# Optimization experiments

Hardware: AMD Instinct MI355X
Metric: run time of the kernel (lower is better)

Reference implementation:

```python
import jax, jax.numpy as jnp
import numpy as np

B, T, I, H = 64, 512, 1024, 1024

def setup_inputs() -> dict:
    key = jax.random.key(0)
    ks = jax.random.split(key, 9)
    def xavier(k, shape):
        bound = np.sqrt(6.0 / (shape[0] + shape[1])).astype(np.float32)
        return jax.random.uniform(k, shape, jnp.float32, -bound, bound)
    inp = {"x": jax.random.normal(ks[0], (B, T, I), jnp.float32)}
    names = ["W_ii", "W_hi", "W_if", "W_hf", "W_ig", "W_hg", "W_io", "W_ho"]
    for n, k in zip(names, ks[1:]):
        rows = I if n[2] == "i" else H
        inp[n] = xavier(k, (rows, H))
    for n in ["b_ii", "b_hi", "b_if", "b_hf", "b_ig", "b_hg", "b_io", "b_ho"]:
        inp[n] = jnp.zeros((H,), jnp.float32)
    return inp

def _lstm(x, W_ii, b_ii, W_hi, b_hi, W_if, b_if, W_hf, b_hf,
          W_ig, b_ig, W_hg, b_hg, W_io, b_io, W_ho, b_ho):
    Bsz, Tlen, _ = x.shape
    Hdim = W_ii.shape[1]
    # Fuse 4 input-side and 4 hidden-side GEMMs into two big ones (same math).
    Wx = jnp.concatenate([W_if, W_ii, W_ig, W_io], axis=1)  # [I, 4H]
    Wh = jnp.concatenate([W_hf, W_hi, W_hg, W_ho], axis=1)  # [H, 4H]
    bsum = jnp.concatenate([b_if + b_hf, b_ii + b_hi, b_ig + b_hg, b_io + b_ho])
    # Hoist the input projection out of the recurrence: [T, B, 4H]
    xg = jnp.swapaxes(jnp.einsum('bti,ig->btg', x, Wx) + bsum, 0, 1)

    def step(carry, g_in):
        h, c = carry
        g = g_in + h @ Wh  # [B, 4H]
        f = jax.nn.sigmoid(g[:, :Hdim])
        i = jax.nn.sigmoid(g[:, Hdim:2 * Hdim])
        gt = jnp.tanh(g[:, 2 * Hdim:3 * Hdim])
        o = jax.nn.sigmoid(g[:, 3 * Hdim:])  # module uses sigmoid_it here
        c_new = f * c + i * gt
        h_new = jnp.tanh(c_new) * o
        return (h_new, c_new), None

    h0 = jnp.zeros((Bsz, Hdim), x.dtype)
    c0 = jnp.zeros((Bsz, Hdim), x.dtype)
    (h_t, c_t), _ = jax.lax.scan(step, (h0, c0), xg)
    return h_t, c_t

def reference(x, W_ii, b_ii, W_hi, b_hi, W_if, b_if, W_hf, b_hf,
              W_ig, b_ig, W_hg, b_hg, W_io, b_io, W_ho, b_ho):
    return _lstm(x, W_ii, b_ii, W_hi, b_hi, W_if, b_if, W_hf, b_hf,
                 W_ig, b_ig, W_hg, b_hg, W_io, b_io, W_ho, b_ho)
```

## Files before the change

### kernel.cpp

```cpp
#include <hip/hip_runtime.h>
#include <hip/hip_bf16.h>

typedef unsigned short u16;
typedef unsigned int   u32;
typedef unsigned long long u64;
typedef short short8 __attribute__((ext_vector_type(8)));
typedef float f32x4  __attribute__((ext_vector_type(4)));
typedef u16   u16x4  __attribute__((ext_vector_type(4)));

#define T_STEPS 512
#define BATCH   64
#define HD      1024
#define NBLK    128
#define NTHR    256
#define NCOL    32
#define WKS     2056
#define HBUF_E  (BATCH * HD)

#define W_BYTES    (NCOL * WKS * 2)
#define G_OFF      W_BYTES
#define G_STRIDE   33
#define G_BYTES    (BATCH * G_STRIDE * 4)
#define B_OFF      (G_OFF + G_BYTES)
#define B_BYTES    (NCOL * 4)
#define F_OFF      (B_OFF + B_BYTES)
#define SMEM_BYTES (F_OFF + 16)

__device__ __forceinline__ float sigm(float x) { return 1.f / (1.f + __expf(-x)); }
__device__ __forceinline__ float tanh_(float x) {
    float ax = __builtin_fabsf(x);
    float e  = __expf(-2.f * ax);
    float r  = (1.f - e) / (1.f + e);
    return x < 0.f ? -r : r;
}
__device__ __forceinline__ short bfb(float f) {
    __hip_bfloat16 h = __float2bfloat16(f);
    return *(short*)&h;
}

__device__ int detect_bf16(const u32* __restrict__ x) {
    int c = 0;
#pragma unroll 8
    for (int i = 0; i < 256; ++i) {
        u32 e = (x[i] >> 7) & 0xFF;
        c += (e >= 100 && e <= 140) ? 1 : 0;
    }
    return c >= 128;
}

extern "C" __global__ void __launch_bounds__(256)
cvt_x_kernel(const void* __restrict__ x, u16* __restrict__ xb, int n4)
{
    __shared__ int flg;
    if (threadIdx.x == 0) flg = detect_bf16((const u32*)x);
    __syncthreads();
    if (flg) return;
    const float4* xf = (const float4*)x;
    u16x4* xo = (u16x4*)xb;
    for (int i = blockIdx.x * blockDim.x + threadIdx.x; i < n4;
         i += gridDim.x * blockDim.x) {
        float4 v = xf[i];
        u16x4 o;
        o[0] = (u16)bfb(v.x); o[1] = (u16)bfb(v.y);
        o[2] = (u16)bfb(v.z); o[3] = (u16)bfb(v.w);
        xo[i] = o;
    }
}

union Frag16 { u64 q[2]; short8 s8[1]; };

__device__ __forceinline__ void load_chunk_atomic(const u16* hp, int c, Frag16* buf) {
#pragma unroll
    for (int it = 0; it < 4; ++it) {
        const u16* ptr = hp + c * 128 + it * 32;
        buf[it].q[0] = __hip_atomic_load((const u64*)ptr, __ATOMIC_RELAXED,
                                         __HIP_MEMORY_SCOPE_AGENT);
        buf[it].q[1] = __hip_atomic_load((const u64*)(ptr + 4), __ATOMIC_RELAXED,
                                         __HIP_MEMORY_SCOPE_AGENT);
    }
}

#define LDX(dst, base, OFFSTR) \
    asm volatile("global_load_dwordx4 %0, %1, off offset:" OFFSTR \
                 : "=v"(dst) : "v"(base))

#define ISSUE_CHUNK(ci) do {                                            \
    const int cc_ = (c0 + (ci)) & 7;                                    \
    u64 bA_ = (u64)(hp + (size_t)cc_ * 8192) + 4096;                    \
    u64 bB_ = bA_ + 8192;                                               \
    LDX(buf[ci][0], bA_, "-4096"); LDX(buf[ci][1], bA_, "0");           \
    LDX(buf[ci][2], bB_, "-4096"); LDX(buf[ci][3], bB_, "0");           \
} while (0)

#define HCHUNK(ci, VMSTR) do {                                          \
    asm volatile("s_waitcnt vmcnt(" VMSTR ")");                         \
    __builtin_amdgcn_sched_barrier(0);                                  \
    const int cc_ = (c0 + (ci)) & 7;                                    \
    const u16* wA_ = wb0 + 1024 + cc_ * 128;                            \
    const u16* wB_ = wb1 + 1024 + cc_ * 128;                            \
    short8 b0_, b1_;                                                    \
    b0_ = *(const short8*)(wA_);       b1_ = *(const short8*)(wB_);     \
    a0 = __builtin_amdgcn_mfma_f32_16x16x32_bf16(buf[ci][0], b0_, a0, 0, 0, 0); \
    a1 = __builtin_amdgcn_mfma_f32_16x16x32_bf16(buf[ci][0], b1_, a1, 0, 0, 0); \
    b0_ = *(const short8*)(wA_ + 32);  b1_ = *(const short8*)(wB_ + 32);\
    a0 = __builtin_amdgcn_mfma_f32_16x16x32_bf16(buf[ci][1], b0_, a0, 0, 0, 0); \
    a1 = __builtin_amdgcn_mfma_f32_16x16x32_bf16(buf[ci][1], b1_, a1, 0, 0, 0); \
    b0_ = *(const short8*)(wA_ + 64);  b1_ = *(const short8*)(wB_ + 64);\
    a0 = __builtin_amdgcn_mfma_f32_16x16x32_bf16(buf[ci][2], b0_, a0, 0, 0, 0); \
    a1 = __builtin_amdgcn_mfma_f32_16x16x32_bf16(buf[ci][2], b1_, a1, 0, 0, 0); \
    b0_ = *(const short8*)(wA_ + 96);  b1_ = *(const short8*)(wB_ + 96);\
    a0 = __builtin_amdgcn_mfma_f32_16x16x32_bf16(buf[ci][3], b0_, a0, 0, 0, 0); \
    a1 = __builtin_amdgcn_mfma_f32_16x16x32_bf16(buf[ci][3], b1_, a1, 0, 0, 0); \
} while (0)

extern "C" __global__ void __launch_bounds__(NTHR, 1)
lstm_persistent(const void* __restrict__ x,
                const void* __restrict__ Wxf, const void* __restrict__ Wxi,
                const void* __restrict__ Wxg, const void* __restrict__ Wxo,
                const void* __restrict__ Whf, const void* __restrict__ Whi,
                const void* __restrict__ Whg, const void* __restrict__ Who,
                const void* __restrict__ bxf, const void* __restrict__ bxi,
                const void* __restrict__ bxg, const void* __restrict__ bxo,
                const void* __restrict__ bhf, const void* __restrict__ bhi,
                const void* __restrict__ bhg, const void* __restrict__ bho,
                u16* __restrict__ hring, int ring_on,
                u16* __restrict__ xb, int* __restrict__ flags,
                void* __restrict__ outv)
{
    __builtin_amdgcn_fence(__ATOMIC_ACQUIRE, "agent");

    extern __shared__ char smem[];
    u16*   w_lds = (u16*)smem;
    float* g_lds = (float*)(smem + G_OFF);
    float* b_lds = (float*)(smem + B_OFF);
    int*   f_lds = (int*)(smem + F_OFF);

    const int tid = threadIdx.x;
    const int blk = blockIdx.x;

    if (tid == 0) f_lds[0] = detect_bf16((const u32*)x);
    __syncthreads();
    const int bf16mode = f_lds[0];

    {
        const int gate = tid >> 6;
        const int kb   = tid & 63;
        const void* WX[4] = {Wxf, Wxi, Wxg, Wxo};
        const void* WH[4] = {Whf, Whi, Whg, Who};
        for (int it = 0; it < 16; ++it) {
            int k = it * 64 + kb;
            u16 vx[8], vh[8];
            if (bf16mode) {
                short8 a = *(const short8*)((const u16*)WX[gate] + (size_t)k * HD + blk * 8);
                short8 b = *(const short8*)((const u16*)WH[gate] + (size_t)k * HD + blk * 8);
#pragma unroll
                for (int ci = 0; ci < 8; ++ci) { vx[ci] = (u16)a[ci]; vh[ci] = (u16)b[ci]; }
            } else {
                const float* px = (const float*)WX[gate] + (size_t)k * HD + blk * 8;
                const float* ph = (const float*)WH[gate] + (size_t)k * HD + blk * 8;
                float4 a0 = *(const float4*)px, a1 = *(const float4*)(px + 4);
                float4 b0 = *(const float4*)ph, b1 = *(const float4*)(ph + 4);
                vx[0]=(u16)bfb(a0.x); vx[1]=(u16)bfb(a0.y); vx[2]=(u16)bfb(a0.z); vx[3]=(u16)bfb(a0.w);
                vx[4]=(u16)bfb(a1.x); vx[5]=(u16)bfb(a1.y); vx[6]=(u16)bfb(a1.z); vx[7]=(u16)bfb(a1.w);
                vh[0]=(u16)bfb(b0.x); vh[1]=(u16)bfb(b0.y); vh[2]=(u16)bfb(b0.z); vh[3]=(u16)bfb(b0.w);
                vh[4]=(u16)bfb(b1.x); vh[5]=(u16)bfb(b1.y); vh[6]=(u16)bfb(b1.z); vh[7]=(u16)bfb(b1.w);
            }
#pragma unroll
            for (int ci = 0; ci < 8; ++ci) {
                w_lds[(gate * 8 + ci) * WKS + k]        = vx[ci];
                w_lds[(gate * 8 + ci) * WKS + 1024 + k] = vh[ci];
            }
        }
    }
    if (tid < NCOL) {
        const void* BX[4] = {bxf, bxi, bxg, bxo};
        const void* BH[4] = {bhf, bhi, bhg, bho};
        int gate = tid >> 3, hc = blk * 8 + (tid & 7);
        float v;
        if (bf16mode)
            v = __bfloat162float(((const __hip_bfloat16*)BX[gate])[hc]) +
                __bfloat162float(((const __hip_bfloat16*)BH[gate])[hc]);
        else
            v = ((const float*)BX[gate])[hc] + ((const float*)BH[gate])[hc];
        b_lds[tid] = v;
    }
    __syncthreads();

    const int wv   = tid >> 6;
    const int lane = tid & 63;
    const int c16  = lane & 15;
    const int quad = lane >> 4;
    const int arow = wv * 16 + c16;

    const int use16 = bf16mode || (xb != nullptr);
    const u16*   x16l = nullptr;
    const float* xf_l = nullptr;
    if (use16) {
        const u16* x16 = bf16mode ? (const u16*)x : xb;
        x16l = x16 + (size_t)arow * T_STEPS * HD + quad * 8;
    } else {
        xf_l = (const float*)x + (size_t)arow * T_STEPS * HD + quad * 8;
    }
    const u16* wb0 = w_lds + c16 * WKS + quad * 8;
    const u16* wb1 = w_lds + (16 + c16) * WKS + quad * 8;

    const int grow = wv * 16 + (lane >> 2);
    const int hl0  = (lane & 3) * 2;
    float bias[8];
#pragma unroll
    for (int g = 0; g < 4; ++g) {
        bias[g * 2]     = b_lds[g * 8 + hl0];
        bias[g * 2 + 1] = b_lds[g * 8 + hl0 + 1];
    }
    float creg[2] = {0.f, 0.f};

    const int c0 = blk >> 4;

    f32x4 ax0 = {0.f,0.f,0.f,0.f}, ax1 = {0.f,0.f,0.f,0.f};
    if (use16) {
        const u16* xp = x16l;
#pragma unroll 8
        for (int kc = 0; kc < 32; ++kc) {
            short8 a  = *(const short8*)(xp + kc * 32);
            short8 b0 = *(const short8*)(wb0 + kc * 32);
            short8 b1 = *(const short8*)(wb1 + kc * 32);
            ax0 = __builtin_amdgcn_mfma_f32_16x16x32_bf16(a, b0, ax0, 0, 0, 0);
            ax1 = __builtin_amdgcn_mfma_f32_16x16x32_bf16(a, b1, ax1, 0, 0, 0);
        }
    } else {
        const float* xp = xf_l;
#pragma unroll 4
        for (int kc = 0; kc < 32; ++kc) {
            float4 fa = *(const float4*)(xp + kc * 32);
            float4 fb = *(const float4*)(xp + kc * 32 + 4);
            short8 a = {bfb(fa.x), bfb(fa.y), bfb(fa.z), bfb(fa.w),
                        bfb(fb.x), bfb(fb.y), bfb(fb.z), bfb(fb.w)};
            short8 b0 = *(const short8*)(wb0 + kc * 32);
            short8 b1 = *(const short8*)(wb1 + kc * 32);
            ax0 = __builtin_amdgcn_mfma_f32_16x16x32_bf16(a, b0, ax0, 0, 0, 0);
            ax1 = __builtin_amdgcn_mfma_f32_16x16x32_bf16(a, b1, ax1, 0, 0, 0);
        }
    }

    for (int t = 0; t < T_STEPS; ++t) {
        f32x4 a0 = ax0, a1 = ax1;

        if (t > 0) {
            while (true) {
                int f1 = __hip_atomic_load(&flags[4 * lane + wv], __ATOMIC_RELAXED,
                                           __HIP_MEMORY_SCOPE_AGENT);
                int f2 = __hip_atomic_load(&flags[256 + 4 * lane + wv], __ATOMIC_RELAXED,
                                           __HIP_MEMORY_SCOPE_AGENT);
                u64 m1 = __ballot(f1 >= t);
                u64 m2 = __ballot(f2 >= t);
                if ((m1 & m2) == ~0ull) break;
                __builtin_amdgcn_s_sleep(1);
            }
            asm volatile("" ::: "memory");

            if (ring_on) {
                const u16* hp = hring + (size_t)(t - 1) * HBUF_E
                              + quad * 512 + arow * 8;
                short8 buf[8][4];
                asm volatile("s_waitcnt vmcnt(0)");
                ISSUE_CHUNK(0); ISSUE_CHUNK(1); ISSUE_CHUNK(2); ISSUE_CHUNK(3);
                ISSUE_CHUNK(4); ISSUE_CHUNK(5); ISSUE_CHUNK(6); ISSUE_CHUNK(7);
                HCHUNK(0, "28"); HCHUNK(1, "24"); HCHUNK(2, "20"); HCHUNK(3, "16");
                HCHUNK(4, "12"); HCHUNK(5, "8");  HCHUNK(6, "4");  HCHUNK(7, "0");
            } else {
                const u16* hp = hring + (size_t)(t & 1) * HBUF_E
                              + (size_t)arow * HD + quad * 8;
                Frag16 bufc[4];
                for (int ci = 0; ci < 8; ++ci) {
                    const int cc = (c0 + ci) & 7;
                    load_chunk_atomic(hp, cc, bufc);
#pragma unroll
                    for (int it = 0; it < 4; ++it) {
                        short8 a  = bufc[it].s8[0];
                        short8 b0 = *(const short8*)(wb0 + 1024 + cc * 128 + it * 32);
                        short8 b1 = *(const short8*)(wb1 + 1024 + cc * 128 + it * 32);
                        a0 = __builtin_amdgcn_mfma_f32_16x16x32_bf16(a, b0, a0, 0, 0, 0);
                        a1 = __builtin_amdgcn_mfma_f32_16x16x32_bf16(a, b1, a1, 0, 0, 0);
                    }
                }
            }
        }

        const int rr = wv * 16 + quad * 4;
#pragma unroll
        for (int i2 = 0; i2 < 4; ++i2) {
            g_lds[(rr + i2) * G_STRIDE + c16]      = a0[i2];
            g_lds[(rr + i2) * G_STRIDE + 16 + c16] = a1[i2];
        }
        asm volatile("s_waitcnt lgkmcnt(0)" ::: "memory");

        float hv[2], cv[2];
#pragma unroll
        for (int jj = 0; jj < 2; ++jj) {
            int hl = hl0 + jj;
            float gf = g_lds[grow * G_STRIDE + hl]      + bias[jj];
            float gi = g_lds[grow * G_STRIDE + 8 + hl]  + bias[2 + jj];
            float gg = g_lds[grow * G_STRIDE + 16 + hl] + bias[4 + jj];
            float go = g_lds[grow * G_STRIDE + 24 + hl] + bias[6 + jj];
            float fg = sigm(gf), ig = sigm(gi), og = sigm(go);
            float gt = tanh_(gg);
            float cnew = fg * creg[jj] + ig * gt;
            creg[jj] = cnew;
            cv[jj] = cnew;
            hv[jj] = tanh_(cnew) * og;
        }

        if (t < T_STEPS - 1) {
            u32 pk = (u32)(u16)bfb(hv[0]) | ((u32)(u16)bfb(hv[1]) << 16);
            if (ring_on) {
                u16* hn = hring + (size_t)t * HBUF_E;
                __hip_atomic_store((u32*)(hn + (size_t)blk * 512 + grow * 8 + hl0),
                                   pk, __ATOMIC_RELAXED, __HIP_MEMORY_SCOPE_AGENT);
            } else {
                u16* hn = hring + (size_t)((t + 1) & 1) * HBUF_E;
                __hip_atomic_store((u32*)(hn + (size_t)grow * HD + blk * 8 + hl0),
                                   pk, __ATOMIC_RELAXED, __HIP_MEMORY_SCOPE_AGENT);
            }
            asm volatile("s_waitcnt vmcnt(0)" ::: "memory");
            if (lane == 0)
                __hip_atomic_store(&flags[4 * blk + wv], t + 1, __ATOMIC_RELAXED,
                                   __HIP_MEMORY_SCOPE_AGENT);

            ax0 = (f32x4){0.f,0.f,0.f,0.f};
            ax1 = (f32x4){0.f,0.f,0.f,0.f};
            if (use16) {
                const u16* xp = x16l + (size_t)(t + 1) * HD;
#pragma unroll 8
                for (int kc = 0; kc < 32; ++kc) {
                    short8 a  = *(const short8*)(xp + kc * 32);
                    short8 b0 = *(const short8*)(wb0 + kc * 32);
                    short8 b1 = *(const short8*)(wb1 + kc * 32);
                    ax0 = __builtin_amdgcn_mfma_f32_16x16x32_bf16(a, b0, ax0, 0, 0, 0);
                    ax1 = __builtin_amdgcn_mfma_f32_16x16x32_bf16(a, b1, ax1, 0, 0, 0);
                }
            } else {
                const float* xp = xf_l + (size_t)(t + 1) * HD;
#pragma unroll 4
                for (int kc = 0; kc < 32; ++kc) {
                    float4 fa = *(const float4*)(xp + kc * 32);
                    float4 fb = *(const float4*)(xp + kc * 32 + 4);
                    short8 a = {bfb(fa.x), bfb(fa.y), bfb(fa.z), bfb(fa.w),
                                bfb(fb.x), bfb(fb.y), bfb(fb.z), bfb(fb.w)};
                    short8 b0 = *(const short8*)(wb0 + kc * 32);
                    short8 b1 = *(const short8*)(wb1 + kc * 32);
                    ax0 = __builtin_amdgcn_mfma_f32_16x16x32_bf16(a, b0, ax0, 0, 0, 0);
                    ax1 = __builtin_amdgcn_mfma_f32_16x16x32_bf16(a, b1, ax1, 0, 0, 0);
                }
            }
        } else {
#pragma unroll
            for (int jj = 0; jj < 2; ++jj) {
                size_t idx = (size_t)grow * HD + blk * 8 + hl0 + jj;
                if (bf16mode) {
                    u16* o = (u16*)outv;
                    __hip_bfloat16 hb = __float2bfloat16(hv[jj]);
                    __hip_bfloat16 cb = __float2bfloat16(cv[jj]);
                    o[idx] = *(u16*)&hb;
                    o[(size_t)BATCH * HD + idx] = *(u16*)&cb;
                } else {
                    float* o = (float*)outv;
                    o[idx] = hv[jj];
                    o[(size_t)BATCH * HD + idx] = cv[jj];
                }
            }
        }
    }
}

extern "C" void kernel_launch(void* const* d_in, const int* in_sizes, int n_in,
                              void* d_out, int out_size, void* d_ws, size_t ws_size,
                              hipStream_t stream) {
    (void)in_sizes; (void)n_in; (void)out_size;
    const void* x   = d_in[0];
    const void* Wii = d_in[1];  const void* Whi = d_in[2];
    const void* Wif = d_in[3];  const void* Whf = d_in[4];
    const void* Wig = d_in[5];  const void* Whg = d_in[6];
    const void* Wio = d_in[7];  const void* Who = d_in[8];
    const void* bii = d_in[9];  const void* bhi = d_in[10];
    const void* bif = d_in[11]; const void* bhf = d_in[12];
    const void* big = d_in[13]; const void* bhg = d_in[14];
    const void* bio = d_in[15]; const void* bho = d_in[16];

    int* flags = (int*)d_ws;
    u16* hring = (u16*)((char*)d_ws + 4096);

    const size_t ring_bytes = (size_t)T_STEPS * HBUF_E * 2;
    const size_t xb_bytes   = (size_t)BATCH * T_STEPS * HD * 2;
    int ring_on = 0;
    u16* xb = nullptr;
    if (ws_size >= 4096 + ring_bytes + xb_bytes) {
        ring_on = 1;
        xb = (u16*)((char*)d_ws + 4096 + ring_bytes);
    } else if (ws_size >= 4096 + ring_bytes) {
        ring_on = 1;
    } else if (ws_size >= 4096 + (size_t)2 * HBUF_E * 2 + xb_bytes) {
        xb = (u16*)((char*)d_ws + 4096 + (size_t)2 * HBUF_E * 2);
    }

    hipMemsetAsync(d_ws, 0, 4096, stream);
    if (xb)
        hipLaunchKernelGGL(cvt_x_kernel, dim3(2048), dim3(256), 0, stream,
                           x, xb, (BATCH * T_STEPS * HD) / 4);

    hipFuncSetAttribute((const void*)lstm_persistent,
                        hipFuncAttributeMaxDynamicSharedMemorySize, SMEM_BYTES);
    hipLaunchKernelGGL(lstm_persistent, dim3(NBLK), dim3(NTHR), SMEM_BYTES, stream,
                       x, Wif, Wii, Wig, Wio, Whf, Whi, Whg, Who,
                       bif, bii, big, bio, bhf, bhi, bhg, bho,
                       hring, ring_on, xb, flags, d_out);
}
```

Before: 4.753 ms.

## Replace flag polling with poisoned-ring data validation for hidden-state sync

In ring mode the per-step flag spin-wait and flag stores are removed. A pre-kernel fills the hidden-state ring with a poison pattern, and consumers speculatively load h chunks, checking each for poison. Clean chunks go straight into the MFMAs, and dirty chunks are reloaded atomically until valid. This takes the flag round-trip off the per-step critical path. The cost is a 64MB poison fill before the kernel, and correctness depends on no valid bf16 pair matching the poison pattern and on 32-bit stores landing atomically.

Measured after the change: 5.822 ms. 1.22x slower.

```diff
diff --git a/kernel.cpp b/kernel.cpp
--- a/kernel.cpp
+++ b/kernel.cpp
@@ -7,6 +7,7 @@
 typedef short short8 __attribute__((ext_vector_type(8)));
 typedef float f32x4  __attribute__((ext_vector_type(4)));
 typedef u16   u16x4  __attribute__((ext_vector_type(4)));
+typedef u32   u32x4  __attribute__((ext_vector_type(4)));
 
 #define T_STEPS 512
 #define BATCH   64
@@ -16,6 +17,7 @@
 #define NCOL    32
 #define WKS     2056
 #define HBUF_E  (BATCH * HD)
+#define POISON  0xFFFFFFFFu
 
 #define W_BYTES    (NCOL * WKS * 2)
 #define G_OFF      W_BYTES
@@ -67,7 +69,17 @@
     }
 }
 
+extern "C" __global__ void __launch_bounds__(256)
+poison_ring_kernel(u32x4* __restrict__ ring, long n)
+{
+    u32x4 p = {POISON, POISON, POISON, POISON};
+    for (long i = (long)blockIdx.x * blockDim.x + threadIdx.x; i < n;
+         i += (long)gridDim.x * blockDim.x)
+        ring[i] = p;
+}
+
 union Frag16 { u64 q[2]; short8 s8[1]; };
+union HF     { short8 s8; u32 w[4]; u64 q[2]; };
 
 __device__ __forceinline__ void load_chunk_atomic(const u16* hp, int c, Frag16* buf) {
 #pragma unroll
@@ -80,6 +92,16 @@
     }
 }
 
+__device__ __forceinline__ int chunk_clean(const HF* b) {
+    u32 ok = 1;
+#pragma unroll
+    for (int it = 0; it < 4; ++it)
+#pragma unroll
+        for (int d = 0; d < 4; ++d)
+            ok &= (b[it].w[d] != POISON) ? 1u : 0u;
+    return __all((int)ok);
+}
+
 #define LDX(dst, base, OFFSTR) \
     asm volatile("global_load_dwordx4 %0, %1, off offset:" OFFSTR \
                  : "=v"(dst) : "v"(base))
@@ -88,29 +110,34 @@
     const int cc_ = (c0 + (ci)) & 7;                                    \
     u64 bA_ = (u64)(hp + (size_t)cc_ * 8192) + 4096;                    \
     u64 bB_ = bA_ + 8192;                                               \
-    LDX(buf[ci][0], bA_, "-4096"); LDX(buf[ci][1], bA_, "0");           \
-    LDX(buf[ci][2], bB_, "-4096"); LDX(buf[ci][3], bB_, "0");           \
+    LDX(buf[ci][0].s8, bA_, "-4096"); LDX(buf[ci][1].s8, bA_, "0");     \
+    LDX(buf[ci][2].s8, bB_, "-4096"); LDX(buf[ci][3].s8, bB_, "0");     \
 } while (0)
 
-#define HCHUNK(ci, VMSTR) do {                                          \
-    asm volatile("s_waitcnt vmcnt(" VMSTR ")");                         \
-    __builtin_amdgcn_sched_barrier(0);                                  \
+#define MFMA_CHUNK(ci) do {                                             \
     const int cc_ = (c0 + (ci)) & 7;                                    \
     const u16* wA_ = wb0 + 1024 + cc_ * 128;                            \
     const u16* wB_ = wb1 + 1024 + cc_ * 128;                            \
     short8 b0_, b1_;                                                    \
     b0_ = *(const short8*)(wA_);       b1_ = *(const short8*)(wB_);     \
-    a0 = __builtin_amdgcn_mfma_f32_16x16x32_bf16(buf[ci][0], b0_, a0, 0, 0, 0); \
-    a1 = __builtin_amdgcn_mfma_f32_16x16x32_bf16(buf[ci][0], b1_, a1, 0, 0, 0); \
+    a0 = __builtin_amdgcn_mfma_f32_16x16x32_bf16(buf[ci][0].s8, b0_, a0, 0, 0, 0); \
+    a1 = __builtin_amdgcn_mfma_f32_16x16x32_bf16(buf[ci][0].s8, b1_, a1, 0, 0, 0); \
     b0_ = *(const short8*)(wA_ + 32);  b1_ = *(const short8*)(wB_ + 32);\
-    a0 = __builtin_amdgcn_mfma_f32_16x16x32_bf16(buf[ci][1], b0_, a0, 0, 0, 0); \
-    a1 = __builtin_amdgcn_mfma_f32_16x16x32_bf16(buf[ci][1], b1_, a1, 0, 0, 0); \
+    a0 = __builtin_amdgcn_mfma_f32_16x16x32_bf16(buf[ci][1].s8, b0_, a0, 0, 0, 0); \
+    a1 = __builtin_amdgcn_mfma_f32_16x16x32_bf16(buf[ci][1].s8, b1_, a1, 0, 0, 0); \
     b0_ = *(const short8*)(wA_ + 64);  b1_ = *(const short8*)(wB_ + 64);\
-    a0 = __builtin_amdgcn_mfma_f32_16x16x32_bf16(buf[ci][2], b0_, a0, 0, 0, 0); \
-    a1 = __builtin_amdgcn_mfma_f32_16x16x32_bf16(buf[ci][2], b1_, a1, 0, 0, 0); \
+    a0 = __builtin_amdgcn_mfma_f32_16x16x32_bf16(buf[ci][2].s8, b0_, a0, 0, 0, 0); \
+    a1 = __builtin_amdgcn_mfma_f32_16x16x32_bf16(buf[ci][2].s8, b1_, a1, 0, 0, 0); \
     b0_ = *(const short8*)(wA_ + 96);  b1_ = *(const short8*)(wB_ + 96);\
-    a0 = __builtin_amdgcn_mfma_f32_16x16x32_bf16(buf[ci][3], b0_, a0, 0, 0, 0); \
-    a1 = __builtin_amdgcn_mfma_f32_16x16x32_bf16(buf[ci][3], b1_, a1, 0, 0, 0); \
+    a0 = __builtin_amdgcn_mfma_f32_16x16x32_bf16(buf[ci][3].s8, b0_, a0, 0, 0, 0); \
+    a1 = __builtin_amdgcn_mfma_f32_16x16x32_bf16(buf[ci][3].s8, b1_, a1, 0, 0, 0); \
+} while (0)
+
+#define HCHK(ci, VMSTR) do {                                            \
+    asm volatile("s_waitcnt vmcnt(" VMSTR ")");                         \
+    __builtin_amdgcn_sched_barrier(0);                                  \
+    if (chunk_clean(buf[ci])) { MFMA_CHUNK(ci); }                       \
+    else { dirty |= (1u << (ci)); }                                     \
 } while (0)
 
 extern "C" __global__ void __launch_bounds__(NTHR, 1)
@@ -246,28 +273,51 @@
         f32x4 a0 = ax0, a1 = ax1;
 
         if (t > 0) {
-            while (true) {
-                int f1 = __hip_atomic_load(&flags[4 * lane + wv], __ATOMIC_RELAXED,
-                                           __HIP_MEMORY_SCOPE_AGENT);
-                int f2 = __hip_atomic_load(&flags[256 + 4 * lane + wv], __ATOMIC_RELAXED,
-                                           __HIP_MEMORY_SCOPE_AGENT);
-                u64 m1 = __ballot(f1 >= t);
-                u64 m2 = __ballot(f2 >= t);
-                if ((m1 & m2) == ~0ull) break;
-                __builtin_amdgcn_s_sleep(1);
-            }
-            asm volatile("" ::: "memory");
-
             if (ring_on) {
                 const u16* hp = hring + (size_t)(t - 1) * HBUF_E
                               + quad * 512 + arow * 8;
-                short8 buf[8][4];
+                HF buf[8][4];
+                u32 dirty = 0;
                 asm volatile("s_waitcnt vmcnt(0)");
                 ISSUE_CHUNK(0); ISSUE_CHUNK(1); ISSUE_CHUNK(2); ISSUE_CHUNK(3);
                 ISSUE_CHUNK(4); ISSUE_CHUNK(5); ISSUE_CHUNK(6); ISSUE_CHUNK(7);
-                HCHUNK(0, "28"); HCHUNK(1, "24"); HCHUNK(2, "20"); HCHUNK(3, "16");
-                HCHUNK(4, "12"); HCHUNK(5, "8");  HCHUNK(6, "4");  HCHUNK(7, "0");
+                HCHK(0, "28"); HCHK(1, "24"); HCHK(2, "20"); HCHK(3, "16");
+                HCHK(4, "12"); HCHK(5, "8");  HCHK(6, "4");  HCHK(7, "0");
+                while (dirty) {
+#pragma unroll
+                    for (int ci = 0; ci < 8; ++ci) {
+                        if (dirty & (1u << ci)) {
+                            const int cc_ = (c0 + ci) & 7;
+#pragma unroll
+                            for (int it = 0; it < 4; ++it) {
+                                const u16* p = hp + (size_t)cc_ * 8192 + it * 2048;
+                                buf[ci][it].q[0] = __hip_atomic_load(
+                                    (const u64*)p, __ATOMIC_RELAXED,
+                                    __HIP_MEMORY_SCOPE_AGENT);
+                                buf[ci][it].q[1] = __hip_atomic_load(
+                                    (const u64*)(p + 4), __ATOMIC_RELAXED,
+                                    __HIP_MEMORY_SCOPE_AGENT);
+                            }
+                            if (chunk_clean(buf[ci])) {
+                                MFMA_CHUNK(ci);
+                                dirty &= ~(1u << ci);
+                            }
+                        }
+                    }
+                    if (dirty) __builtin_amdgcn_s_sleep(1);
+                }
             } else {
+                while (true) {
+                    int f1 = __hip_atomic_load(&flags[4 * lane + wv], __ATOMIC_RELAXED,
+                                               __HIP_MEMORY_SCOPE_AGENT);
+                    int f2 = __hip_atomic_load(&flags[256 + 4 * lane + wv], __ATOMIC_RELAXED,
+                                               __HIP_MEMORY_SCOPE_AGENT);
+                    u64 m1 = __ballot(f1 >= t);
+                    u64 m2 = __ballot(f2 >= t);
+                    if ((m1 & m2) == ~0ull) break;
+                    __builtin_amdgcn_s_sleep(1);
+                }
+                asm volatile("" ::: "memory");
                 const u16* hp = hring + (size_t)(t & 1) * HBUF_E
                               + (size_t)arow * HD + quad * 8;
                 Frag16 bufc[4];
@@ -320,11 +370,11 @@
                 u16* hn = hring + (size_t)((t + 1) & 1) * HBUF_E;
                 __hip_atomic_store((u32*)(hn + (size_t)grow * HD + blk * 8 + hl0),
                                    pk, __ATOMIC_RELAXED, __HIP_MEMORY_SCOPE_AGENT);
-            }
-            asm volatile("s_waitcnt vmcnt(0)" ::: "memory");
-            if (lane == 0)
-                __hip_atomic_store(&flags[4 * blk + wv], t + 1, __ATOMIC_RELAXED,
-                                   __HIP_MEMORY_SCOPE_AGENT);
+                asm volatile("s_waitcnt vmcnt(0)" ::: "memory");
+                if (lane == 0)
+                    __hip_atomic_store(&flags[4 * blk + wv], t + 1, __ATOMIC_RELAXED,
+                                       __HIP_MEMORY_SCOPE_AGENT);
+            }
 
             ax0 = (f32x4){0.f,0.f,0.f,0.f};
             ax1 = (f32x4){0.f,0.f,0.f,0.f};
@@ -406,6 +456,9 @@
     if (xb)
         hipLaunchKernelGGL(cvt_x_kernel, dim3(2048), dim3(256), 0, stream,
                            x, xb, (BATCH * T_STEPS * HD) / 4);
+    if (ring_on)
+        hipLaunchKernelGGL(poison_ring_kernel, dim3(2048), dim3(256), 0, stream,
+                           (u32x4*)hring, (long)(ring_bytes / 16));
 
     hipFuncSetAttribute((const void*)lstm_persistent,
                         hipFuncAttributeMaxDynamicSharedMemorySize, SMEM_BYTES);
```
